# Performance work log

Hardware: AMD Instinct MI355X
Metric: run time of the kernel (lower is better)

The kernel has to match this reference:

```python
import jax, jax.numpy as jnp
import numpy as np

N = 512          # data_info['n']
K = 513          # data_info['k'] + 1
B = 65536        # batch size


def _build_adjust(n, k):
    # Reproduces the __init__ mask construction exactly.
    a1 = np.ones((n - 1, k - 1, 2), dtype=np.float32)
    a2 = np.zeros((n - 1, k - 1, 2), dtype=np.float32)
    for i in range(0, k - 2):
        if i >= n - 1:
            break
        f1 = a1[i].reshape(-1)
        f1[2 + 2 * i:] = 0
        a1[i] = f1.reshape(k - 1, 2)
        f2 = a2[i].reshape(-1)
        f2[2 + 2 * i + 1] = 1
        a2[i] = f2.reshape(k - 1, 2)
    return jnp.asarray(a1), jnp.asarray(a2)


W_ADJ1, W_ADJ2 = _build_adjust(N, K)


def setup_inputs() -> dict:
    key = jax.random.key(0)
    k1, k2, k3 = jax.random.split(key, 3)
    x = jax.random.randint(k1, (B, N), 0, 2, dtype=jnp.int32)
    W = jax.random.normal(k2, (N - 1, K - 1, 2), dtype=jnp.float32)
    endW = jax.random.normal(k3, (1, K), dtype=jnp.float32)
    return {"x": x, "W": W, "endW": endW}


def reference(x, W, endW):
    # W_full construction (softmax over the 2-way split, masked, with the
    # deterministic [1,0] row prepended along the group axis).
    Wsm = jax.nn.softmax(W, axis=2)                      # (n-1, k-1, 2)
    W_full = Wsm * W_ADJ1 + W_ADJ2                       # (n-1, k-1, 2)
    append = jnp.zeros((N - 1, 1, 2), W_full.dtype).at[:, :, 0].set(1.0)
    W_full = jnp.concatenate([append, W_full], axis=1)   # (n-1, k, 2)

    # group_num at step i is the running cumsum of x[:, 0..i]; the serial
    # recurrence collapses to a single cumsum, letting us gather all steps
    # at once instead of the original n-1 step Python loop.
    g = jnp.cumsum(x, axis=1)                            # (B, n)
    steps = jnp.arange(N - 1)                            # step i -> W_full[i-1]
    vals = W_full[steps[None, :], g[:, 1:], x[:, 1:]]    # (B, n-1)
    out = jnp.sum(jnp.log(vals), axis=1, keepdims=True)  # (B, 1)

    e = jax.nn.softmax(endW, axis=1)[0]                  # (k,)
    out = out + jnp.log(e[g[:, -1]])[:, None]            # (B, 1)
    return out
```

## Files before the change

kernel.cpp:

```cpp
#include <hip/hip_runtime.h>
#include <math.h>

#define NN      512
#define KK      513
#define BB      65536
#define TROWS   512
#define TCOLS   513
#define T16STR  528

#define BLK     256

typedef int iv4 __attribute__((ext_vector_type(4)));

__device__ __forceinline__ unsigned f2bf(float f) {
    unsigned u = __float_as_uint(f);
    return (u + 0x7fffu + ((u >> 16) & 1u)) >> 16;
}

__global__ void build_table_kernel(const float* __restrict__ W, const float* __restrict__ endW,
                                   unsigned* __restrict__ T16, float* __restrict__ logE) {
    int idx = blockIdx.x * blockDim.x + threadIdx.x;
    if (idx < TROWS * TCOLS) {
        int t = idx / TCOLS;
        int g = idx - t * TCOLS;
        float v0 = 0.f, v1 = 0.f;
        if (t >= 1 && g >= 1 && g <= t) {
            const float* w = W + ((size_t)(t - 1) * (KK - 1) + (g - 1)) * 2;
            float w0 = w[0], w1 = w[1];
            float m  = fmaxf(w0, w1);
            float lse = m + __logf(__expf(w0 - m) + __expf(w1 - m));
            v0 = w0 - lse;
            v1 = w1 - lse;
        }
        T16[t * T16STR + g] = f2bf(v0) | (f2bf(v1) << 16);
    }
    if (blockIdx.x == 0 && threadIdx.x < 64) {
        int lane = threadIdx.x;
        float vals[9];
        float m = -1e30f;
        #pragma unroll
        for (int k = 0; k < 9; ++k) {
            int i = lane + 64 * k;
            vals[k] = (i < KK) ? endW[i] : -1e30f;
            m = fmaxf(m, vals[k]);
        }
        #pragma unroll
        for (int d = 32; d >= 1; d >>= 1) m = fmaxf(m, __shfl_xor(m, d, 64));
        float s = 0.f;
        #pragma unroll
        for (int k = 0; k < 9; ++k) s += __expf(vals[k] - m);
        #pragma unroll
        for (int d = 32; d >= 1; d >>= 1) s += __shfl_xor(s, d, 64);
        float lse = m + __logf(s);
        #pragma unroll
        for (int k = 0; k < 9; ++k) {
            int i = lane + 64 * k;
            if (i < KK) logE[i] = endW[i] - lse;
        }
    }
}

__global__ __launch_bounds__(BLK, 8) void pc_main_kernel(
    const int* __restrict__ x, const unsigned* __restrict__ T16,
    const float* __restrict__ logE, float* __restrict__ out)
{
    __shared__ unsigned xposed[4 * 128];

    const int tid  = threadIdx.x;
    const int wid  = tid >> 6;
    const int lane = tid & 63;
    const int gw   = blockIdx.x * 4 + wid;
    const int ridx = lane & 7;
    const int s    = lane >> 3;

    const iv4* xt = (const iv4*)(x + (size_t)gw * (8 * NN));
    unsigned p0 = 0, p1 = 0;
    {
        iv4 A[8];
        #pragma unroll
        for (int j = 0; j < 8; ++j) A[j] = __builtin_nontemporal_load(&xt[j * 64 + lane]);
        #pragma unroll
        for (int j = 0; j < 8; ++j) {
            unsigned nib = (unsigned)(A[j].x & 1) | ((unsigned)(A[j].y & 1) << 1)
                         | ((unsigned)(A[j].z & 1) << 2) | ((unsigned)(A[j].w & 1) << 3);
            p0 |= nib << (4 * j);
        }
        #pragma unroll
        for (int j = 0; j < 8; ++j) A[j] = __builtin_nontemporal_load(&xt[(8 + j) * 64 + lane]);
        #pragma unroll
        for (int j = 0; j < 8; ++j) {
            unsigned nib = (unsigned)(A[j].x & 1) | ((unsigned)(A[j].y & 1) << 1)
                         | ((unsigned)(A[j].z & 1) << 2) | ((unsigned)(A[j].w & 1) << 3);
            p1 |= nib << (4 * j);
        }
    }

    unsigned* wb = &xposed[wid * 128];
    wb[lane]      = p0;
    wb[64 + lane] = p1;
    __builtin_amdgcn_sched_barrier(0);

    const unsigned base  = ((ridx < 4) ? 0u : 64u) + 16u * (s & 3);
    const int      shift = 4 * ((2 * ridx + (s >> 2)) & 7);
    unsigned lo = 0, hi = 0;
    #pragma unroll
    for (int m = 0; m < 8; ++m)  lo |= ((wb[base + m] >> shift) & 0xFu) << (4 * m);
    #pragma unroll
    for (int m = 8; m < 16; ++m) hi |= ((wb[base + m] >> shift) & 0xFu) << (4 * (m - 8));

    int pc  = __popc(lo) + __popc(hi);
    int inc = pc, t1;
    t1 = __shfl_up(inc, 8,  64); if (s >= 1) inc += t1;
    t1 = __shfl_up(inc, 16, 64); if (s >= 2) inc += t1;
    t1 = __shfl_up(inc, 32, 64); if (s >= 4) inc += t1;
    int g = inc - pc;

    float a0 = 0.f, a1 = 0.f, a2 = 0.f, a3 = 0.f;
    const unsigned* Ts = T16 + (size_t)(64 * s) * T16STR;
    #pragma unroll
    for (int k = 0; k < 32; ++k) {
        int b = (lo >> k) & 1; g += b;
        unsigned u = Ts[k * T16STR + g];
        float v = __uint_as_float(b ? (u & 0xffff0000u) : (u << 16));
        if      ((k & 3) == 0) a0 += v;
        else if ((k & 3) == 1) a1 += v;
        else if ((k & 3) == 2) a2 += v;
        else                   a3 += v;
    }
    #pragma unroll
    for (int k = 0; k < 32; ++k) {
        int b = (hi >> k) & 1; g += b;
        unsigned u = Ts[(32 + k) * T16STR + g];
        float v = __uint_as_float(b ? (u & 0xffff0000u) : (u << 16));
        if      ((k & 3) == 0) a0 += v;
        else if ((k & 3) == 1) a1 += v;
        else if ((k & 3) == 2) a2 += v;
        else                   a3 += v;
    }

    float part = (a0 + a1) + (a2 + a3);
    part += __shfl_xor(part, 8,  64);
    part += __shfl_xor(part, 16, 64);
    part += __shfl_xor(part, 32, 64);
    if (s == 7)
        out[gw * 8 + ridx] = part + logE[inc];
}

extern "C" void kernel_launch(void* const* d_in, const int* in_sizes, int n_in,
                              void* d_out, int out_size, void* d_ws, size_t ws_size,
                              hipStream_t stream)
{
    const int*   x    = (const int*)d_in[0];
    const float* W    = (const float*)d_in[1];
    const float* endW = (const float*)d_in[2];
    float*       out  = (float*)d_out;

    unsigned* T16  = (unsigned*)d_ws;
    float*    logE = (float*)((char*)d_ws + (size_t)TROWS * T16STR * sizeof(unsigned));

    {
        int total  = TROWS * TCOLS;
        int blocks = (total + BLK - 1) / BLK;
        build_table_kernel<<<blocks, BLK, 0, stream>>>(W, endW, T16, logE);
    }
    pc_main_kernel<<<BB / (8 * 4), BLK, 0, stream>>>(x, T16, logE, out);
}
```

Measured before the change: 211.3 us.

## Restructure main kernel into block-level tiles with double-buffered x prefetch

The main kernel now has each 256-thread block process two 32-row tiles. The x tile is packed into padded shared memory, and the block-wide prefix of bit counts is computed through shared segment sums instead of wave shuffles. The global loads for the second tile are issued in the middle of the first tile's table-gather loop, so memory latency overlaps with compute. All 64 table loads are issued ahead of the accumulation. This raises register use (launch bounds drop to 4 blocks per CU), adds __syncthreads, and halves the grid size.

New measurement: 194.2 us, median of 2. -8.1%, faster.

```diff
diff --git a/kernel.cpp b/kernel.cpp
--- a/kernel.cpp
+++ b/kernel.cpp
@@ -8,7 +8,11 @@
 #define TCOLS   513
 #define T16STR  528
 
+#define TILE_R  32
+#define TPB     2
 #define BLK     256
+#define XSTR    129
+#define TILE_I4 (TILE_R * NN / 4)
 
 typedef int iv4 __attribute__((ext_vector_type(4)));
 
@@ -60,90 +64,113 @@
     }
 }
 
-__global__ __launch_bounds__(BLK, 8) void pc_main_kernel(
+__global__ __launch_bounds__(BLK, 4) void pc_main_kernel(
     const int* __restrict__ x, const unsigned* __restrict__ T16,
     const float* __restrict__ logE, float* __restrict__ out)
 {
-    __shared__ unsigned xposed[4 * 128];
+    __shared__ unsigned xb[2][TILE_R * XSTR];
+    __shared__ int      segsum[8 * TILE_R];
+    __shared__ float    partial[8 * TILE_R];
 
     const int tid  = threadIdx.x;
-    const int wid  = tid >> 6;
-    const int lane = tid & 63;
-    const int gw   = blockIdx.x * 4 + wid;
-    const int ridx = lane & 7;
-    const int s    = lane >> 3;
+    const int r    = tid & 31;
+    const int s    = tid >> 5;
+    const int row0 = blockIdx.x * (TILE_R * TPB);
 
-    const iv4* xt = (const iv4*)(x + (size_t)gw * (8 * NN));
-    unsigned p0 = 0, p1 = 0;
-    {
-        iv4 A[8];
+    const iv4* tb = (const iv4*)(x + (size_t)row0 * NN);
+
+    iv4 A[16];
+    #pragma unroll
+    for (int j = 0; j < 16; ++j) A[j] = __builtin_nontemporal_load(&tb[tid + BLK * j]);
+    #pragma unroll
+    for (int j = 0; j < 16; ++j) {
+        int i = tid + BLK * j;
+        unsigned m = (unsigned)(A[j].x & 1) | ((unsigned)(A[j].y & 1) << 8)
+                   | ((unsigned)(A[j].z & 1) << 16) | ((unsigned)(A[j].w & 1) << 24);
+        xb[0][(i >> 7) * XSTR + (i & 127)] = m;
+    }
+    __syncthreads();
+
+    #pragma unroll
+    for (int t = 0; t < TPB; ++t) {
+        unsigned w[16];
+        int ssum = 0;
         #pragma unroll
-        for (int j = 0; j < 8; ++j) A[j] = __builtin_nontemporal_load(&xt[j * 64 + lane]);
+        for (int m = 0; m < 16; ++m) {
+            w[m] = xb[t][r * XSTR + s * 16 + m];
+            ssum += __popc(w[m]);
+        }
+        segsum[s * TILE_R + r] = ssum;
+        __syncthreads();
+
+        int g = 0, gtot = 0;
         #pragma unroll
-        for (int j = 0; j < 8; ++j) {
-            unsigned nib = (unsigned)(A[j].x & 1) | ((unsigned)(A[j].y & 1) << 1)
-                         | ((unsigned)(A[j].z & 1) << 2) | ((unsigned)(A[j].w & 1) << 3);
-            p0 |= nib << (4 * j);
+        for (int q = 0; q < 8; ++q) {
+            int v = segsum[q * TILE_R + r];
+            if (q < s) g += v;
+            gtot += v;
         }
+
+        unsigned u[64];
+        const unsigned* Ts = T16 + (size_t)(s * 64) * T16STR;
         #pragma unroll
-        for (int j = 0; j < 8; ++j) A[j] = __builtin_nontemporal_load(&xt[(8 + j) * 64 + lane]);
+        for (int m = 0; m < 16; ++m) {
+            #pragma unroll
+            for (int q = 0; q < 4; ++q) {
+                int b = (w[m] >> (8 * q)) & 1;
+                g += b;
+                u[4 * m + q] = Ts[(4 * m + q) * T16STR + g];
+            }
+        }
+
+        float a0 = 0.f, a1 = 0.f, a2 = 0.f, a3 = 0.f;
         #pragma unroll
-        for (int j = 0; j < 8; ++j) {
-            unsigned nib = (unsigned)(A[j].x & 1) | ((unsigned)(A[j].y & 1) << 1)
-                         | ((unsigned)(A[j].z & 1) << 2) | ((unsigned)(A[j].w & 1) << 3);
-            p1 |= nib << (4 * j);
+        for (int k = 0; k < 48; ++k) {
+            int b = (w[k >> 2] >> (8 * (k & 3))) & 1;
+            float v = __uint_as_float(b ? (u[k] & 0xffff0000u) : (u[k] << 16));
+            if      ((k & 3) == 0) a0 += v;
+            else if ((k & 3) == 1) a1 += v;
+            else if ((k & 3) == 2) a2 += v;
+            else                   a3 += v;
+        }
+
+        if (t + 1 < TPB) {
+            __builtin_amdgcn_sched_barrier(0);
+            #pragma unroll
+            for (int j = 0; j < 16; ++j)
+                A[j] = __builtin_nontemporal_load(&tb[TILE_I4 + tid + BLK * j]);
+            __builtin_amdgcn_sched_barrier(0);
+        }
+
+        #pragma unroll
+        for (int k = 48; k < 64; ++k) {
+            int b = (w[k >> 2] >> (8 * (k & 3))) & 1;
+            float v = __uint_as_float(b ? (u[k] & 0xffff0000u) : (u[k] << 16));
+            if      ((k & 3) == 0) a0 += v;
+            else if ((k & 3) == 1) a1 += v;
+            else if ((k & 3) == 2) a2 += v;
+            else                   a3 += v;
+        }
+        partial[s * TILE_R + r] = (a0 + a1) + (a2 + a3);
+
+        if (t + 1 < TPB) {
+            #pragma unroll
+            for (int j = 0; j < 16; ++j) {
+                int i = tid + BLK * j;
+                unsigned m = (unsigned)(A[j].x & 1) | ((unsigned)(A[j].y & 1) << 8)
+                           | ((unsigned)(A[j].z & 1) << 16) | ((unsigned)(A[j].w & 1) << 24);
+                xb[t + 1][(i >> 7) * XSTR + (i & 127)] = m;
+            }
+        }
+        __syncthreads();
+
+        if (s == 0) {
+            float o = logE[gtot];
+            #pragma unroll
+            for (int q = 0; q < 8; ++q) o += partial[q * TILE_R + r];
+            out[row0 + t * TILE_R + r] = o;
         }
     }
-
-    unsigned* wb = &xposed[wid * 128];
-    wb[lane]      = p0;
-    wb[64 + lane] = p1;
-    __builtin_amdgcn_sched_barrier(0);
-
-    const unsigned base  = ((ridx < 4) ? 0u : 64u) + 16u * (s & 3);
-    const int      shift = 4 * ((2 * ridx + (s >> 2)) & 7);
-    unsigned lo = 0, hi = 0;
-    #pragma unroll
-    for (int m = 0; m < 8; ++m)  lo |= ((wb[base + m] >> shift) & 0xFu) << (4 * m);
-    #pragma unroll
-    for (int m = 8; m < 16; ++m) hi |= ((wb[base + m] >> shift) & 0xFu) << (4 * (m - 8));
-
-    int pc  = __popc(lo) + __popc(hi);
-    int inc = pc, t1;
-    t1 = __shfl_up(inc, 8,  64); if (s >= 1) inc += t1;
-    t1 = __shfl_up(inc, 16, 64); if (s >= 2) inc += t1;
-    t1 = __shfl_up(inc, 32, 64); if (s >= 4) inc += t1;
-    int g = inc - pc;
-
-    float a0 = 0.f, a1 = 0.f, a2 = 0.f, a3 = 0.f;
-    const unsigned* Ts = T16 + (size_t)(64 * s) * T16STR;
-    #pragma unroll
-    for (int k = 0; k < 32; ++k) {
-        int b = (lo >> k) & 1; g += b;
-        unsigned u = Ts[k * T16STR + g];
-        float v = __uint_as_float(b ? (u & 0xffff0000u) : (u << 16));
-        if      ((k & 3) == 0) a0 += v;
-        else if ((k & 3) == 1) a1 += v;
-        else if ((k & 3) == 2) a2 += v;
-        else                   a3 += v;
-    }
-    #pragma unroll
-    for (int k = 0; k < 32; ++k) {
-        int b = (hi >> k) & 1; g += b;
-        unsigned u = Ts[(32 + k) * T16STR + g];
-        float v = __uint_as_float(b ? (u & 0xffff0000u) : (u << 16));
-        if      ((k & 3) == 0) a0 += v;
-        else if ((k & 3) == 1) a1 += v;
-        else if ((k & 3) == 2) a2 += v;
-        else                   a3 += v;
-    }
-
-    float part = (a0 + a1) + (a2 + a3);
-    part += __shfl_xor(part, 8,  64);
-    part += __shfl_xor(part, 16, 64);
-    part += __shfl_xor(part, 32, 64);
-    if (s == 7)
-        out[gw * 8 + ridx] = part + logE[inc];
 }
 
 extern "C" void kernel_launch(void* const* d_in, const int* in_sizes, int n_in,
@@ -163,5 +190,5 @@
         int blocks = (total + BLK - 1) / BLK;
         build_table_kernel<<<blocks, BLK, 0, stream>>>(W, endW, T16, logE);
     }
-    pc_main_kernel<<<BB / (8 * 4), BLK, 0, stream>>>(x, T16, logE, out);
+    pc_main_kernel<<<BB / (TILE_R * TPB), BLK, 0, stream>>>(x, T16, logE, out);
 }
```
